# Performance work log

Measured on AMD Instinct MI355X. Metric: run time of the kernel, lower is better.

The kernel has to match this reference:

```python
import jax, jax.numpy as jnp
import numpy as np

BN_EPS = 1e-5

def gin_layer(x, src, dst, w1, b1, w2, b2, gamma, beta):
    # GINConv with eps=0: h_i = MLP(x_i + sum_{j->i} x_j)
    agg = jax.ops.segment_sum(x[src], dst, num_segments=x.shape[0])  # [N, D]
    h = x + agg
    h = jnp.maximum(h @ w1 + b1, 0.0) @ w2 + b2
    # BatchNorm (training-mode batch statistics, biased var as in torch)
    mu = jnp.mean(h, axis=0)
    var = jnp.var(h, axis=0)
    h = (h - mu) * jax.lax.rsqrt(var + BN_EPS) * gamma + beta
    return jnp.maximum(h, 0.0)  # ReLU (dropout = identity in eval)

def setup_inputs() -> dict:
    key = jax.random.key(0)
    N, E, G = 20000, 320000, 64
    dims = [128, 128, 256, 512]
    ks = jax.random.split(key, 32)
    inp = {
        "x": jax.random.normal(ks[0], (N, dims[0]), dtype=jnp.float32),
        "edge_index": jax.random.randint(ks[1], (2, E), 0, N, dtype=jnp.int64),
        "batch_idx": jnp.sort(jax.random.randint(ks[2], (N,), 0, G, dtype=jnp.int64)),
    }
    ki = 3
    for li, (di, do) in enumerate(zip(dims[:-1], dims[1:])):
        s = chr(ord('a') + li)
        inp[f"w1{s}"] = jax.random.normal(ks[ki], (di, do), dtype=jnp.float32) * (1.0 / np.sqrt(di)); ki += 1
        inp[f"b1{s}"] = jnp.zeros((do,), dtype=jnp.float32)
        inp[f"w2{s}"] = jax.random.normal(ks[ki], (do, do), dtype=jnp.float32) * (1.0 / np.sqrt(do)); ki += 1
        inp[f"b2{s}"] = jnp.zeros((do,), dtype=jnp.float32)
        inp[f"gn{s}"] = jnp.ones((do,), dtype=jnp.float32)
        inp[f"bn{s}"] = jnp.zeros((do,), dtype=jnp.float32)
    inp["wo"] = jax.random.normal(ks[ki], (dims[-1], 64), dtype=jnp.float32) * (1.0 / np.sqrt(dims[-1]))
    inp["bo"] = jnp.zeros((64,), dtype=jnp.float32)
    return inp

def reference(x, edge_index, batch_idx,
              w1a, b1a, w2a, b2a, gna, bna,
              w1b, b1b, w2b, b2b, gnb, bnb,
              w1c, b1c, w2c, b2c, gnc, bnc,
              wo, bo):
    G = 64
    src, dst = edge_index[0], edge_index[1]
    h = gin_layer(x, src, dst, w1a, b1a, w2a, b2a, gna, bna)
    h = gin_layer(h, src, dst, w1b, b1b, w2b, b2b, gnb, bnb)
    h = gin_layer(h, src, dst, w1c, b1c, w2c, b2c, gnc, bnc)
    # global mean pool over graphs
    sums = jax.ops.segment_sum(h, batch_idx, num_segments=G)  # [G, 512]
    cnts = jax.ops.segment_sum(jnp.ones((h.shape[0],), h.dtype), batch_idx, num_segments=G)
    pooled = sums / jnp.maximum(cnts, 1.0)[:, None]
    # output projection: Linear -> ReLU (dropout identity in eval)
    return jnp.maximum(pooled @ wo + bo, 0.0)
```

## Files before the change

kernel.cpp:

```cpp
#include <hip/hip_runtime.h>

typedef float f32x4 __attribute__((ext_vector_type(4)));
typedef _Float16 f16x2 __attribute__((ext_vector_type(2)));
typedef _Float16 f16x4 __attribute__((ext_vector_type(4)));
typedef _Float16 f16x8 __attribute__((ext_vector_type(8)));

__global__ __launch_bounds__(256) void hist_kernel(const int* __restrict__ dst,
                                                   int* __restrict__ deg, int E) {
  int e = blockIdx.x * 256 + threadIdx.x;
  if (e < E) atomicAdd(&deg[dst[e]], 1);
}

__global__ __launch_bounds__(1024) void scan_kernel(const int* __restrict__ deg,
                                                    int* __restrict__ rowstart,
                                                    int* __restrict__ cursor, int N) {
  __shared__ int sums[1024];
  const int t = threadIdx.x;
  const int CH = (N + 1023) >> 10;
  int local[32];
  int base = t * CH;
  int s = 0;
  for (int i = 0; i < CH; i++) {
    int idx = base + i;
    int v = (idx < N) ? deg[idx] : 0;
    local[i] = s;
    s += v;
  }
  sums[t] = s;
  __syncthreads();
  for (int off = 1; off < 1024; off <<= 1) {
    int add = (t >= off) ? sums[t - off] : 0;
    __syncthreads();
    sums[t] += add;
    __syncthreads();
  }
  int prefix = sums[t] - s;
  for (int i = 0; i < CH; i++) {
    int idx = base + i;
    if (idx < N) {
      int v = prefix + local[i];
      rowstart[idx] = v;
      cursor[idx] = v;
    }
  }
  if (t == 1023) rowstart[N] = sums[1023];
}

__global__ __launch_bounds__(256) void fill_kernel(const int* __restrict__ src,
                                                   const int* __restrict__ dst,
                                                   int* __restrict__ cursor,
                                                   int* __restrict__ nbr, int E) {
  int e = blockIdx.x * 256 + threadIdx.x;
  if (e >= E) return;
  int pos = atomicAdd(&cursor[dst[e]], 1);
  nbr[pos] = src[e];
}

__global__ __launch_bounds__(256) void xprep_kernel(const float4* __restrict__ in,
                                                    f16x4* __restrict__ out, int n4) {
  int i = blockIdx.x * 256 + threadIdx.x;
  if (i >= n4) return;
  float4 v = in[i];
  f16x4 h;
  h[0] = (_Float16)v.x; h[1] = (_Float16)v.y;
  h[2] = (_Float16)v.z; h[3] = (_Float16)v.w;
  out[i] = h;
}

template <int C, bool BNIN>
__global__ __launch_bounds__(256) void gather_agg_kernel(
    const _Float16* __restrict__ x, const int* __restrict__ rowstart,
    const int* __restrict__ nbr, const float* __restrict__ stats,
    const float* __restrict__ gamma, const float* __restrict__ beta,
    _Float16* __restrict__ agg, int N, float invN) {
  constexpr int Din = 64 * C;
  const int wave = threadIdx.x >> 6;
  const int lane = threadIdx.x & 63;
  const int node = blockIdx.x * 4 + wave;
  if (node >= N) return;

  float sc[C], sh[C];
  if constexpr (BNIN) {
#pragma unroll
    for (int j = 0; j < C; j++) {
      int c = lane * C + j;
      float mean = stats[c] * invN;
      float var = stats[Din + c] * invN - mean * mean;
      sc[j] = rsqrtf(var + 1e-5f) * gamma[c];
      sh[j] = beta[c] - mean * sc[j];
    }
  }

#define LOADROW(dstv, rowidx)                                              \
  {                                                                        \
    const _Float16* _p = x + (size_t)(rowidx)*Din + lane * C;              \
    if constexpr (C == 2) {                                                \
      f16x2 _t = *(const f16x2*)_p;                                        \
      dstv[0] = (float)_t[0]; dstv[1] = (float)_t[1];                      \
    } else {                                                               \
      f16x4 _t = *(const f16x4*)_p;                                        \
      dstv[0] = (float)_t[0]; dstv[1] = (float)_t[1];                      \
      dstv[2] = (float)_t[2]; dstv[3] = (float)_t[3];                      \
    }                                                                      \
  }
#define ACCUM(vv)                                                          \
  _Pragma("unroll") for (int j = 0; j < C; j++)                            \
      acc[j] += BNIN ? fmaxf(vv[j] * sc[j] + sh[j], 0.f) : vv[j];

  float acc[C];
  {
    float v[C];
    LOADROW(v, node)
#pragma unroll
    for (int j = 0; j < C; j++)
      acc[j] = BNIN ? fmaxf(v[j] * sc[j] + sh[j], 0.f) : v[j];
  }
  const int rs = rowstart[node], re = rowstart[node + 1];
  int e = rs;
  for (; e + 3 < re; e += 4) {
    int s0 = nbr[e], s1 = nbr[e + 1], s2 = nbr[e + 2], s3 = nbr[e + 3];
    float v0[C], v1[C], v2[C], v3[C];
    LOADROW(v0, s0)
    LOADROW(v1, s1)
    LOADROW(v2, s2)
    LOADROW(v3, s3)
    ACCUM(v0) ACCUM(v1) ACCUM(v2) ACCUM(v3)
  }
  for (; e + 1 < re; e += 2) {
    int s0 = nbr[e], s1 = nbr[e + 1];
    float v0[C], v1[C];
    LOADROW(v0, s0)
    LOADROW(v1, s1)
    ACCUM(v0) ACCUM(v1)
  }
  if (e < re) {
    int s0 = nbr[e];
    float v0[C];
    LOADROW(v0, s0)
    ACCUM(v0)
  }
#undef ACCUM
#undef LOADROW

  _Float16* o = agg + (size_t)node * Din + lane * C;
  if constexpr (C == 2) {
    f16x2 r; r[0] = (_Float16)acc[0]; r[1] = (_Float16)acc[1];
    *(f16x2*)o = r;
  } else {
    f16x4 r;
    r[0] = (_Float16)acc[0]; r[1] = (_Float16)acc[1];
    r[2] = (_Float16)acc[2]; r[3] = (_Float16)acc[3];
    *(f16x4*)o = r;
  }
}

struct WSeg {
  const float* W;
  _Float16* TH;
  int K, N, total;
};
struct WAll { WSeg s[6]; };

__global__ __launch_bounds__(256) void wprep_all_kernel(WAll a) {
  WSeg sg = a.s[blockIdx.y];
  int idx = blockIdx.x * 256 + threadIdx.x;
  if (idx >= sg.total) return;
  int k = idx / sg.N, n = idx - k * sg.N;
  sg.TH[(size_t)n * sg.K + k] = (_Float16)sg.W[idx];
}

template <int RT>
__global__ __launch_bounds__(256, 8) void gemm_mfma_kernel(
    const _Float16* __restrict__ A, const _Float16* __restrict__ BT,
    const float* __restrict__ bias, _Float16* __restrict__ Ch,
    int M, int K, int N, int mblocks, int cbShift,
    int doRelu, float* __restrict__ stats) {
  constexpr int NF = RT / 16;
  constexpr int NP = RT / 32;
  __shared__ _Float16 Ah[2 * NF * 512];
  const int bid = blockIdx.x;
  const int xcd = bid & 7;
  const int q = bid >> 3;
  const int r = ((q >> cbShift) << 3) + xcd;
  const int cb = q & ((1 << cbShift) - 1);
  if (r >= mblocks) return;

  const int tid = threadIdx.x;
  const int lane = tid & 63;
  const int w = tid >> 6;
  const int rowBase = r * RT;
  const int colBase = cb * 128 + w * 32;

  f32x4 acc[NF][2] = {};

  const int c0 = colBase + (lane & 15);
  const int kfrag = (lane >> 4) * 8;

  int srow, slane, sfrag0, kk0;
  if constexpr (RT == 64) {
    srow = tid >> 2;
    const int schunk = tid & 3;
    slane = (srow & 15) | (schunk << 4);
    sfrag0 = srow >> 4;
    kk0 = schunk * 8;
  } else {
    srow = tid >> 3;
    const int c8 = tid & 7;
    const int lc = c8 & 3, ks = c8 >> 2;
    slane = (srow & 15) | (lc << 4);
    sfrag0 = ks * NF + (srow >> 4);
    kk0 = lc * 8 + ks * 32;
  }
  const size_t arowOff = (size_t)(rowBase + srow) * K;
  const bool srowOk = (rowBase + srow) < M;

  for (int k0 = 0; k0 < K; k0 += 64) {
#pragma unroll
    for (int i = 0; i < NP; i++) {
      int kk = k0 + kk0 + (RT == 64 ? i * 32 : 0);
      f16x8 h8 = {};
      if (srowOk) h8 = *(const f16x8*)(A + arowOff + kk);
      int frag = (RT == 64 ? i * NF + sfrag0 : sfrag0);
      *(f16x8*)(Ah + frag * 512 + slane * 8) = h8;
    }
    __syncthreads();
#pragma unroll
    for (int ks = 0; ks < 2; ks++) {
      int kidx = k0 + ks * 32 + kfrag;
      f16x8 bh0 = *(const f16x8*)(BT + (size_t)c0 * K + kidx);
      f16x8 bh1 = *(const f16x8*)(BT + (size_t)(c0 + 16) * K + kidx);
#pragma unroll
      for (int fi = 0; fi < NF; fi++) {
        int frag = ks * NF + fi;
        f16x8 ah = *(const f16x8*)(Ah + frag * 512 + lane * 8);
        acc[fi][0] = __builtin_amdgcn_mfma_f32_16x16x32_f16(ah, bh0, acc[fi][0], 0, 0, 0);
        acc[fi][1] = __builtin_amdgcn_mfma_f32_16x16x32_f16(ah, bh1, acc[fi][1], 0, 0, 0);
      }
    }
    __syncthreads();
  }

  const float bias0 = bias[c0], bias1 = bias[c0 + 16];
  float s1[2] = {0.f, 0.f}, s2[2] = {0.f, 0.f};
  const int rbase = rowBase + (lane >> 4) * 4;
#pragma unroll
  for (int fi = 0; fi < NF; fi++) {
#pragma unroll
    for (int j = 0; j < 4; j++) {
      int row = rbase + fi * 16 + j;
      float v0 = acc[fi][0][j] + bias0;
      float v1 = acc[fi][1][j] + bias1;
      if (doRelu) { v0 = fmaxf(v0, 0.f); v1 = fmaxf(v1, 0.f); }
      if (row < M) {
        Ch[(size_t)row * N + c0] = (_Float16)v0;
        Ch[(size_t)row * N + c0 + 16] = (_Float16)v1;
        s1[0] += v0; s2[0] += v0 * v0;
        s1[1] += v1; s2[1] += v1 * v1;
      }
    }
  }
  if (stats) {
#pragma unroll
    for (int off = 16; off < 64; off <<= 1) {
      s1[0] += __shfl_xor(s1[0], off);
      s2[0] += __shfl_xor(s2[0], off);
      s1[1] += __shfl_xor(s1[1], off);
      s2[1] += __shfl_xor(s2[1], off);
    }
    if (lane < 16) {
      atomicAdd(&stats[c0], s1[0]);
      atomicAdd(&stats[N + c0], s2[0]);
      atomicAdd(&stats[c0 + 16], s1[1]);
      atomicAdd(&stats[N + c0 + 16], s2[1]);
    }
  }
}

__global__ __launch_bounds__(256) void bn_pool_kernel(
    const _Float16* __restrict__ h, const float* __restrict__ stats,
    const float* __restrict__ gamma, const float* __restrict__ beta,
    const int* __restrict__ batch, float* __restrict__ pooled, int N, float invN) {
  const int g = blockIdx.x >> 3;
  const int s = blockIdx.x & 7;
  __shared__ int s_lo, s_hi;
  if (threadIdx.x == 0) {
    int lo = 0, hi = N;
    while (lo < hi) { int m = (lo + hi) >> 1; if (batch[m] < g) lo = m + 1; else hi = m; }
    s_lo = lo;
    lo = 0; hi = N;
    while (lo < hi) { int m = (lo + hi) >> 1; if (batch[m] < g + 1) lo = m + 1; else hi = m; }
    s_hi = lo;
  }
  __syncthreads();
  const int lo = s_lo, hi = s_hi, len = hi - lo;
  if (len == 0) return;
  const int per = (len + 7) >> 3;
  const int rs = lo + s * per;
  const int re = min(rs + per, hi);
  if (rs >= re) return;
  const int t = threadIdx.x;
  float scv[2], shv[2];
#pragma unroll
  for (int j = 0; j < 2; j++) {
    int c = 2 * t + j;
    float mean = stats[c] * invN;
    float var = stats[512 + c] * invN - mean * mean;
    scv[j] = rsqrtf(var + 1e-5f) * gamma[c];
    shv[j] = beta[c] - mean * scv[j];
  }
  float ax = 0.f, ay = 0.f;
  for (int r = rs; r < re; r++) {
    f16x2 v = *(const f16x2*)(h + (size_t)r * 512 + 2 * t);
    ax += fmaxf((float)v[0] * scv[0] + shv[0], 0.f);
    ay += fmaxf((float)v[1] * scv[1] + shv[1], 0.f);
  }
  float inv = 1.f / (float)len;
  atomicAdd(&pooled[g * 512 + 2 * t], ax * inv);
  atomicAdd(&pooled[g * 512 + 2 * t + 1], ay * inv);
}

__global__ __launch_bounds__(64) void out_kernel(const float* __restrict__ pooled,
                                                 const float* __restrict__ wo,
                                                 const float* __restrict__ bo,
                                                 float* __restrict__ out) {
  int g = blockIdx.x, o = threadIdx.x;
  float acc = bo[o];
  for (int c = 0; c < 512; c++) acc += pooled[g * 512 + c] * wo[c * 64 + o];
  out[g * 64 + o] = fmaxf(acc, 0.f);
}

extern "C" void kernel_launch(void* const* d_in, const int* in_sizes, int n_in,
                              void* d_out, int out_size, void* d_ws, size_t ws_size,
                              hipStream_t stream) {
  const float* x0 = (const float*)d_in[0];
  const int* ei = (const int*)d_in[1];
  const int* batch = (const int*)d_in[2];
  const int N = in_sizes[0] / 128;
  const int E = in_sizes[1] / 2;
  const int* src = ei;
  const int* dst = ei + E;
  const float* W[3][6];
  for (int li = 0; li < 3; li++)
    for (int k = 0; k < 6; k++) W[li][k] = (const float*)d_in[3 + li * 6 + k];
  const float* wo = (const float*)d_in[21];
  const float* bo = (const float*)d_in[22];
  float* out = (float*)d_out;

  float* stats3 = (float*)d_ws;
  float* pooled = stats3 + 3 * 1024;
  int* deg = (int*)(pooled + 64 * 512);
  int* rowstart = deg + N;
  int* cursor = rowstart + N + 1;
  int* nbr = cursor + N;
  uintptr_t wp = (uintptr_t)(nbr + E);
  wp = (wp + 15) & ~(uintptr_t)15;
  _Float16* aggh = (_Float16*)wp;
  _Float16* h1h = aggh + (size_t)N * 256;
  _Float16* h2h = h1h + (size_t)N * 512;
  _Float16* x0h = h2h + (size_t)N * 512;
  _Float16* wbuf = x0h + (size_t)N * 128;

  const int dins[3] = {128, 128, 256};
  const int douts[3] = {128, 256, 512};

  _Float16* WT[3][2];
  {
    _Float16* p = wbuf;
    for (int li = 0; li < 3; li++) {
      WT[li][0] = p; p += (size_t)dins[li] * douts[li];
      WT[li][1] = p; p += (size_t)douts[li] * douts[li];
    }
  }
  {
    WAll wa;
    int maxTotal = 0;
    for (int li = 0; li < 3; li++) {
      int e1 = dins[li] * douts[li];
      int e2 = douts[li] * douts[li];
      wa.s[li * 2 + 0] = WSeg{W[li][0], WT[li][0], dins[li], douts[li], e1};
      wa.s[li * 2 + 1] = WSeg{W[li][2], WT[li][1], douts[li], douts[li], e2};
      maxTotal = max(maxTotal, max(e1, e2));
    }
    dim3 g((maxTotal + 255) / 256, 6);
    wprep_all_kernel<<<g, 256, 0, stream>>>(wa);
  }

  {
    int n4 = N * 32;
    xprep_kernel<<<(n4 + 255) / 256, 256, 0, stream>>>((const float4*)x0, (f16x4*)x0h, n4);
  }

  hipMemsetAsync(deg, 0, (size_t)N * sizeof(int), stream);
  hist_kernel<<<(E + 255) / 256, 256, 0, stream>>>(dst, deg, E);
  scan_kernel<<<1, 1024, 0, stream>>>(deg, rowstart, cursor, N);
  fill_kernel<<<(E + 255) / 256, 256, 0, stream>>>(src, dst, cursor, nbr, E);

  hipMemsetAsync(stats3, 0, (3 * 1024 + 64 * 512) * sizeof(float), stream);

  const int mb64 = (N + 63) / 64;
  const int mb64_8 = ((mb64 + 7) / 8) * 8;
  const int mb32 = (N + 31) / 32;
  const int mb32_8 = ((mb32 + 7) / 8) * 8;
  const int gblocks = (N + 3) / 4;
  const float invN = 1.0f / N;

  for (int li = 0; li < 3; li++) {
    int Din = dins[li], Dout = douts[li];
    float* stats = stats3 + li * 1024;
    if (li == 0)
      gather_agg_kernel<2, false><<<gblocks, 256, 0, stream>>>(
          x0h, rowstart, nbr, nullptr, nullptr, nullptr, aggh, N, invN);
    else if (li == 1)
      gather_agg_kernel<2, true><<<gblocks, 256, 0, stream>>>(
          h2h, rowstart, nbr, stats3 + 0 * 1024, W[0][4], W[0][5], aggh, N, invN);
    else
      gather_agg_kernel<4, true><<<gblocks, 256, 0, stream>>>(
          h2h, rowstart, nbr, stats3 + 1 * 1024, W[1][4], W[1][5], aggh, N, invN);

    if (Dout == 128) {
      gemm_mfma_kernel<32><<<mb32_8, 256, 0, stream>>>(aggh, WT[li][0], W[li][1], h1h,
                                                       N, Din, Dout, mb32, 0, 1, nullptr);
      gemm_mfma_kernel<32><<<mb32_8, 256, 0, stream>>>(h1h, WT[li][1], W[li][3], h2h,
                                                       N, Dout, Dout, mb32, 0, 0, stats);
    } else {
      int cbShift = (Dout == 256) ? 1 : 2;
      int nblocks = mb64_8 << cbShift;
      gemm_mfma_kernel<64><<<nblocks, 256, 0, stream>>>(aggh, WT[li][0], W[li][1], h1h,
                                                        N, Din, Dout, mb64, cbShift, 1, nullptr);
      gemm_mfma_kernel<64><<<nblocks, 256, 0, stream>>>(h1h, WT[li][1], W[li][3], h2h,
                                                        N, Dout, Dout, mb64, cbShift, 0, stats);
    }
    if (li == 2) {
      bn_pool_kernel<<<64 * 8, 256, 0, stream>>>(
          h2h, stats3 + 2 * 1024, W[2][4], W[2][5], batch, pooled, N, invN);
    }
  }
  out_kernel<<<64, 64, 0, stream>>>(pooled, wo, bo, out);
}
```

Measured before the change: 289.3 us.

## Double-buffer GEMM A tiles via direct global-to-LDS loads; fold memsets into xprep

The MFMA GEMM now stages A tiles straight into LDS using global_load_lds and double-buffers them, so the load of the next K-slice overlaps the MFMAs on the current one. Rows past M are clamped to M-1 instead of zero-filled, which is harmless because those rows are masked on store. The two hipMemsetAsync calls that zeroed the degree and stats buffers are folded into the xprep kernel to save launches. The cost is twice the LDS per block, which may lower occupancy, and possible ordering hazards because the async LDS writes rely only on __syncthreads with no explicit vmcnt wait.

```diff
diff --git a/kernel.cpp b/kernel.cpp
--- a/kernel.cpp
+++ b/kernel.cpp
@@ -4,6 +4,12 @@
 typedef _Float16 f16x2 __attribute__((ext_vector_type(2)));
 typedef _Float16 f16x4 __attribute__((ext_vector_type(4)));
 typedef _Float16 f16x8 __attribute__((ext_vector_type(8)));
+
+__device__ __forceinline__ void gload_lds16(const _Float16* g, _Float16* l) {
+  __builtin_amdgcn_global_load_lds(
+      (const __attribute__((address_space(1))) unsigned int*)g,
+      (__attribute__((address_space(3))) unsigned int*)l, 16, 0, 0);
+}
 
 __global__ __launch_bounds__(256) void hist_kernel(const int* __restrict__ dst,
                                                    int* __restrict__ deg, int E) {
@@ -57,8 +63,12 @@
 }
 
 __global__ __launch_bounds__(256) void xprep_kernel(const float4* __restrict__ in,
-                                                    f16x4* __restrict__ out, int n4) {
+                                                    f16x4* __restrict__ out, int n4,
+                                                    int* __restrict__ deg, int N,
+                                                    float* __restrict__ zbuf, int zn) {
   int i = blockIdx.x * 256 + threadIdx.x;
+  if (i < N) deg[i] = 0;
+  if (i < zn) zbuf[i] = 0.f;
   if (i >= n4) return;
   float4 v = in[i];
   f16x4 h;
@@ -176,8 +186,9 @@
     int M, int K, int N, int mblocks, int cbShift,
     int doRelu, float* __restrict__ stats) {
   constexpr int NF = RT / 16;
-  constexpr int NP = RT / 32;
-  __shared__ _Float16 Ah[2 * NF * 512];
+  constexpr int NFT = 2 * NF;
+  constexpr int FPW = NFT / 4;
+  __shared__ _Float16 Ah[2][NFT * 512];
   const int bid = blockIdx.x;
   const int xcd = bid & 7;
   const int q = bid >> 3;
@@ -192,53 +203,50 @@
   const int colBase = cb * 128 + w * 32;
 
   f32x4 acc[NF][2] = {};
-
   const int c0 = colBase + (lane & 15);
   const int kfrag = (lane >> 4) * 8;
 
-  int srow, slane, sfrag0, kk0;
-  if constexpr (RT == 64) {
-    srow = tid >> 2;
-    const int schunk = tid & 3;
-    slane = (srow & 15) | (schunk << 4);
-    sfrag0 = srow >> 4;
-    kk0 = schunk * 8;
-  } else {
-    srow = tid >> 3;
-    const int c8 = tid & 7;
-    const int lc = c8 & 3, ks = c8 >> 2;
-    slane = (srow & 15) | (lc << 4);
-    sfrag0 = ks * NF + (srow >> 4);
-    kk0 = lc * 8 + ks * 32;
-  }
-  const size_t arowOff = (size_t)(rowBase + srow) * K;
-  const bool srowOk = (rowBase + srow) < M;
-
-  for (int k0 = 0; k0 < K; k0 += 64) {
-#pragma unroll
-    for (int i = 0; i < NP; i++) {
-      int kk = k0 + kk0 + (RT == 64 ? i * 32 : 0);
-      f16x8 h8 = {};
-      if (srowOk) h8 = *(const f16x8*)(A + arowOff + kk);
-      int frag = (RT == 64 ? i * NF + sfrag0 : sfrag0);
-      *(f16x8*)(Ah + frag * 512 + slane * 8) = h8;
-    }
-    __syncthreads();
+  size_t srcOff[FPW];
+#pragma unroll
+  for (int i = 0; i < FPW; i++) {
+    int F = w * FPW + i;
+    int ks = F / NF, fi = F % NF;
+    int row = rowBase + fi * 16 + (lane & 15);
+    row = min(row, M - 1);
+    srcOff[i] = (size_t)row * K + ks * 32 + ((lane >> 4) << 3);
+  }
+
+#define STAGE(b, t)                                                        \
+  {                                                                        \
+    _Pragma("unroll") for (int i = 0; i < FPW; i++)                        \
+        gload_lds16(A + srcOff[i] + (size_t)(t) * 64,                      \
+                    Ah[b] + (w * FPW + i) * 512);                          \
+  }
+
+  const int NT = K >> 6;
+  STAGE(0, 0)
+  __syncthreads();
+  int cur = 0;
+  for (int t = 0; t < NT; t++) {
+    if (t + 1 < NT) {
+      if (cur) STAGE(0, t + 1) else STAGE(1, t + 1)
+    }
 #pragma unroll
     for (int ks = 0; ks < 2; ks++) {
-      int kidx = k0 + ks * 32 + kfrag;
+      int kidx = t * 64 + ks * 32 + kfrag;
       f16x8 bh0 = *(const f16x8*)(BT + (size_t)c0 * K + kidx);
       f16x8 bh1 = *(const f16x8*)(BT + (size_t)(c0 + 16) * K + kidx);
 #pragma unroll
       for (int fi = 0; fi < NF; fi++) {
-        int frag = ks * NF + fi;
-        f16x8 ah = *(const f16x8*)(Ah + frag * 512 + lane * 8);
+        f16x8 ah = *(const f16x8*)(Ah[cur] + (ks * NF + fi) * 512 + lane * 8);
         acc[fi][0] = __builtin_amdgcn_mfma_f32_16x16x32_f16(ah, bh0, acc[fi][0], 0, 0, 0);
         acc[fi][1] = __builtin_amdgcn_mfma_f32_16x16x32_f16(ah, bh1, acc[fi][1], 0, 0, 0);
       }
     }
     __syncthreads();
-  }
+    cur ^= 1;
+  }
+#undef STAGE
 
   const float bias0 = bias[c0], bias1 = bias[c0 + 16];
   float s1[2] = {0.f, 0.f}, s2[2] = {0.f, 0.f};
@@ -387,15 +395,14 @@
 
   {
     int n4 = N * 32;
-    xprep_kernel<<<(n4 + 255) / 256, 256, 0, stream>>>((const float4*)x0, (f16x4*)x0h, n4);
-  }
-
-  hipMemsetAsync(deg, 0, (size_t)N * sizeof(int), stream);
+    int zn = 3 * 1024 + 64 * 512;
+    xprep_kernel<<<(n4 + 255) / 256, 256, 0, stream>>>(
+        (const float4*)x0, (f16x4*)x0h, n4, deg, N, stats3, zn);
+  }
+
   hist_kernel<<<(E + 255) / 256, 256, 0, stream>>>(dst, deg, E);
   scan_kernel<<<1, 1024, 0, stream>>>(deg, rowstart, cursor, N);
   fill_kernel<<<(E + 255) / 256, 256, 0, stream>>>(src, dst, cursor, nbr, E);
-
-  hipMemsetAsync(stats3, 0, (3 * 1024 + 64 * 512) * sizeof(float), stream);
 
   const int mb64 = (N + 63) / 64;
   const int mb64_8 = ((mb64 + 7) / 8) * 8;
```

Result: no change. 290.4 us (+0.4%).
